# Performance work log

Hardware: AMD Instinct MI355X
Metric: run time of the kernel (lower is better)

Reference implementation:

```python
import jax, jax.numpy as jnp
import numpy as np

D_MODEL = 1024
NUM_HEADS = 16
HEAD_DIM = D_MODEL // NUM_HEADS


def setup_inputs() -> dict:
    key = jax.random.key(0)
    ks = jax.random.split(key, 11)
    B, S = 2, 2048
    s = 1.0 / np.sqrt(D_MODEL)
    return {
        "q": jax.random.normal(ks[0], (B, S, D_MODEL), jnp.float32),
        "k": jax.random.normal(ks[1], (B, S, D_MODEL), jnp.float32),
        "v": jax.random.normal(ks[2], (B, S, D_MODEL), jnp.float32),
        "Wq": jax.random.normal(ks[3], (D_MODEL, D_MODEL), jnp.float32) * s,
        "bq": jnp.zeros((D_MODEL,), jnp.float32),
        "Wk": jax.random.normal(ks[4], (D_MODEL, D_MODEL), jnp.float32) * s,
        "bk": jnp.zeros((D_MODEL,), jnp.float32),
        "Wv": jax.random.normal(ks[5], (D_MODEL, D_MODEL), jnp.float32) * s,
        "bv": jnp.zeros((D_MODEL,), jnp.float32),
        "Wo": jax.random.normal(ks[6], (D_MODEL, D_MODEL), jnp.float32) * s,
        "bo": jnp.zeros((D_MODEL,), jnp.float32),
    }


def _split_heads(x):
    B, S, _ = x.shape
    return x.reshape(B, S, NUM_HEADS, HEAD_DIM).transpose(0, 2, 1, 3)  # [B,H,S,Dh]


def reference(q, k, v, Wq, bq, Wk, bk, Wv, bv, Wo, bo):
    B, S, _ = q.shape
    qh = _split_heads(q @ Wq.T + bq)
    kh = _split_heads(k @ Wk.T + bk)
    vh = _split_heads(v @ Wv.T + bv)
    scale = 1.0 / jnp.sqrt(jnp.asarray(HEAD_DIM, qh.dtype))
    scores = jnp.einsum("bhqd,bhkd->bhqk", qh, kh) * scale  # [B,H,S,S]
    attn = jax.nn.softmax(scores, axis=-1)
    out = jnp.einsum("bhqk,bhkd->bhqd", attn, vh)
    out = out.transpose(0, 2, 1, 3).reshape(B, S, D_MODEL)
    return out @ Wo.T + bo
```

## Files before the change

kernel.cpp:

```cpp
#include <hip/hip_runtime.h>
#include <cstdint>
#include <cstddef>

#define DEVI __device__ __forceinline__

typedef short bf16x8 __attribute__((ext_vector_type(8)));
typedef short bf16x4 __attribute__((ext_vector_type(4)));
typedef float f32x4 __attribute__((ext_vector_type(4)));
typedef float f32x16 __attribute__((ext_vector_type(16)));
typedef unsigned short u16x4 __attribute__((ext_vector_type(4)));

constexpr int D_MODEL = 1024;
constexpr int HEADS = 16;
constexpr int DH = 64;
constexpr int SEQ = 2048;
constexpr int KDIM = 1024;

DEVI unsigned short f2bf(float f) {
  union { float f; unsigned u; } v; v.f = f;
  unsigned r = v.u + 0x7fffu + ((v.u >> 16) & 1u);
  return (unsigned short)(r >> 16);
}

DEVI unsigned pkbf(float a, float b) {
  return __builtin_amdgcn_perm(__float_as_uint(b), __float_as_uint(a), 0x07060302u);
}

DEVI void cp16(const void* g, void* l) {
  __builtin_amdgcn_global_load_lds(
      (const __attribute__((address_space(1))) void*)g,
      (__attribute__((address_space(3))) void*)l, 16, 0, 0);
}

#define BAR()        asm volatile("s_barrier" ::: "memory")
#define WAITVM(n)    asm volatile("s_waitcnt vmcnt(" #n ")" ::: "memory")

__global__ void __launch_bounds__(256) castall(
    const float* __restrict__ q, const float* __restrict__ k, const float* __restrict__ v,
    const float* __restrict__ Wq, const float* __restrict__ Wk,
    const float* __restrict__ Wv, const float* __restrict__ Wo,
    unsigned short* __restrict__ qb, unsigned short* __restrict__ kb, unsigned short* __restrict__ vb,
    unsigned short* __restrict__ Wqb, unsigned short* __restrict__ Wkb,
    unsigned short* __restrict__ Wvb, unsigned short* __restrict__ Wob) {
  int bid = blockIdx.x;
  const float* s; unsigned short* d; int off;
  if (bid < 12288) {
    int w = bid >> 12; off = bid & 4095;
    s = (w == 0) ? q : ((w == 1) ? k : v);
    d = (w == 0) ? qb : ((w == 1) ? kb : vb);
  } else {
    int w = (bid - 12288) >> 10; off = bid & 1023;
    s = (w == 0) ? Wq : ((w == 1) ? Wk : ((w == 2) ? Wv : Wo));
    d = (w == 0) ? Wqb : ((w == 1) ? Wkb : ((w == 2) ? Wvb : Wob));
  }
  int i = (off * 256 + threadIdx.x) * 4;
  float4 x = *(const float4*)(s + i);
  u16x4 o; o[0] = f2bf(x.x); o[1] = f2bf(x.y); o[2] = f2bf(x.z); o[3] = f2bf(x.w);
  *(u16x4*)(d + i) = o;
}

__global__ void __launch_bounds__(256) qkv_gemm(
    const unsigned short* __restrict__ qb, const unsigned short* __restrict__ kb,
    const unsigned short* __restrict__ vb,
    const unsigned short* __restrict__ Wqb, const unsigned short* __restrict__ Wkb,
    const unsigned short* __restrict__ Wvb,
    const float* __restrict__ bq, const float* __restrict__ bk, const float* __restrict__ bv,
    unsigned short* __restrict__ Qh, unsigned short* __restrict__ Kh,
    unsigned short* __restrict__ Vt, float qscale) {
  __shared__ unsigned short As[3][128 * 32];
  __shared__ unsigned short Bs[3][128 * 32];
  const int bid = blockIdx.x, seg = bid >> 8, inner = bid & 255;
  const int bm = inner & 31, bn = inner >> 5;
  const unsigned short* A = (seg == 0) ? qb : ((seg == 1) ? kb : vb);
  const unsigned short* W = (seg == 0) ? Wqb : ((seg == 1) ? Wkb : Wvb);
  const float* bias = (seg == 0) ? bq : ((seg == 1) ? bk : bv);
  unsigned short* O = (seg == 0) ? Qh : ((seg == 1) ? Kh : Vt);
  const float oscale = (seg == 0) ? qscale : 1.0f;
  const int mode = (seg == 2) ? 1 : 0;

  const int tid = threadIdx.x, lane = tid & 63, wave = tid >> 6;
  const int l16 = lane & 15, quad = lane >> 4;
  const int wm = (wave >> 1) * 64, wn = (wave & 1) * 64;
  const int sw = (l16 >> 1) & 3;
  f32x4 acc[4][4] = {};

  const int r0 = tid >> 2, p0 = tid & 3;
  const int c0 = (p0 ^ ((r0 >> 1) & 3)) * 8;
  const int r1 = (256 + tid) >> 2;
  const int c1 = (p0 ^ ((r1 >> 1) & 3)) * 8;
  const unsigned short* Arow0 = A + (size_t)(bm * 128 + r0) * KDIM + c0;
  const unsigned short* Arow1 = A + (size_t)(bm * 128 + r1) * KDIM + c1;
  const unsigned short* Wrow0 = W + (size_t)(bn * 128 + r0) * KDIM + c0;
  const unsigned short* Wrow1 = W + (size_t)(bn * 128 + r1) * KDIM + c1;

#define QKV_ISSUE(K0, P)                                    \
  do {                                                      \
    cp16(Arow0 + (K0), &As[P][tid * 8]);                    \
    cp16(Arow1 + (K0), &As[P][(256 + tid) * 8]);            \
    cp16(Wrow0 + (K0), &Bs[P][tid * 8]);                    \
    cp16(Wrow1 + (K0), &Bs[P][(256 + tid) * 8]);            \
  } while (0)

#define QKV_COMPUTE(P)                                                             \
  do {                                                                             \
    bf16x8 af[4], bfr[4];                                                          \
    _Pragma("unroll") for (int t = 0; t < 4; ++t)                                  \
        af[t] = *(const bf16x8*)&As[P][(wm + t * 16 + l16) * 32 + ((quad ^ sw) * 8)]; \
    _Pragma("unroll") for (int t = 0; t < 4; ++t)                                  \
        bfr[t] = *(const bf16x8*)&Bs[P][(wn + t * 16 + l16) * 32 + ((quad ^ sw) * 8)]; \
    _Pragma("unroll") for (int i = 0; i < 4; ++i)                                  \
        _Pragma("unroll") for (int j = 0; j < 4; ++j)                              \
            acc[i][j] = __builtin_amdgcn_mfma_f32_16x16x32_bf16(af[i], bfr[j],     \
                                                                acc[i][j], 0, 0, 0); \
  } while (0)

  QKV_ISSUE(0, 0);
  QKV_ISSUE(32, 1);
  for (int k = 0; k < 30; k += 3) {
    BAR(); QKV_ISSUE((k + 2) * 32, 2); WAITVM(8); BAR(); QKV_COMPUTE(0);
    BAR(); QKV_ISSUE((k + 3) * 32, 0); WAITVM(8); BAR(); QKV_COMPUTE(1);
    BAR(); QKV_ISSUE((k + 4) * 32, 1); WAITVM(8); BAR(); QKV_COMPUTE(2);
  }
  WAITVM(4); BAR(); QKV_COMPUTE(0);
  WAITVM(0); BAR(); QKV_COMPUTE(1);

#pragma unroll
  for (int i = 0; i < 4; ++i) {
#pragma unroll
    for (int j = 0; j < 4; ++j) {
      const int col = bn * 128 + wn + j * 16 + l16;
      const float bv = bias[col];
#pragma unroll
      for (int r = 0; r < 4; ++r) {
        const int row = bm * 128 + wm + i * 16 + quad * 4 + r;
        const float val = (acc[i][j][r] + bv) * oscale;
        const int b = row >> 11, s = row & (SEQ - 1);
        const int h = col >> 6, d = col & (DH - 1);
        size_t idx;
        if (mode == 0) idx = ((size_t)(b * HEADS + h) * SEQ + s) * DH + d;
        else           idx = ((size_t)(b * HEADS + h) * DH + d) * SEQ + s;
        O[idx] = f2bf(val);
      }
    }
  }
#undef QKV_ISSUE
#undef QKV_COMPUTE
}

__global__ void __launch_bounds__(256) out_gemm(const unsigned short* __restrict__ AO,
                                                const unsigned short* __restrict__ Wob,
                                                const float* __restrict__ bo,
                                                float* __restrict__ out) {
  __shared__ unsigned short As[3][128 * 32];
  __shared__ unsigned short Bs[3][128 * 32];
  const int bid = blockIdx.x, bm = bid & 31, bn = bid >> 5;
  const int tid = threadIdx.x, lane = tid & 63, wave = tid >> 6;
  const int l16 = lane & 15, quad = lane >> 4;
  const int wm = (wave >> 1) * 64, wn = (wave & 1) * 64;
  const int sw = (l16 >> 1) & 3;
  f32x4 acc[4][4] = {};

  const int r0 = tid >> 2, p0 = tid & 3;
  const int c0 = (p0 ^ ((r0 >> 1) & 3)) * 8;
  const int r1 = (256 + tid) >> 2;
  const int c1 = (p0 ^ ((r1 >> 1) & 3)) * 8;
  const unsigned short* Arow0 = AO + (size_t)(bm * 128 + r0) * KDIM + c0;
  const unsigned short* Arow1 = AO + (size_t)(bm * 128 + r1) * KDIM + c1;
  const unsigned short* Wrow0 = Wob + (size_t)(bn * 128 + r0) * KDIM + c0;
  const unsigned short* Wrow1 = Wob + (size_t)(bn * 128 + r1) * KDIM + c1;

#define OUT_ISSUE(K0, P)                                    \
  do {                                                      \
    cp16(Arow0 + (K0), &As[P][tid * 8]);                    \
    cp16(Arow1 + (K0), &As[P][(256 + tid) * 8]);            \
    cp16(Wrow0 + (K0), &Bs[P][tid * 8]);                    \
    cp16(Wrow1 + (K0), &Bs[P][(256 + tid) * 8]);            \
  } while (0)

#define OUT_COMPUTE(P)                                                             \
  do {                                                                             \
    bf16x8 af[4], bfr[4];                                                          \
    _Pragma("unroll") for (int t = 0; t < 4; ++t)                                  \
        af[t] = *(const bf16x8*)&As[P][(wm + t * 16 + l16) * 32 + ((quad ^ sw) * 8)]; \
    _Pragma("unroll") for (int t = 0; t < 4; ++t)                                  \
        bfr[t] = *(const bf16x8*)&Bs[P][(wn + t * 16 + l16) * 32 + ((quad ^ sw) * 8)]; \
    _Pragma("unroll") for (int i = 0; i < 4; ++i)                                  \
        _Pragma("unroll") for (int j = 0; j < 4; ++j)                              \
            acc[i][j] = __builtin_amdgcn_mfma_f32_16x16x32_bf16(af[i], bfr[j],     \
                                                                acc[i][j], 0, 0, 0); \
  } while (0)

  OUT_ISSUE(0, 0);
  OUT_ISSUE(32, 1);
  for (int k = 0; k < 30; k += 3) {
    BAR(); OUT_ISSUE((k + 2) * 32, 2); WAITVM(8); BAR(); OUT_COMPUTE(0);
    BAR(); OUT_ISSUE((k + 3) * 32, 0); WAITVM(8); BAR(); OUT_COMPUTE(1);
    BAR(); OUT_ISSUE((k + 4) * 32, 1); WAITVM(8); BAR(); OUT_COMPUTE(2);
  }
  WAITVM(4); BAR(); OUT_COMPUTE(0);
  WAITVM(0); BAR(); OUT_COMPUTE(1);

#pragma unroll
  for (int i = 0; i < 4; ++i)
#pragma unroll
    for (int j = 0; j < 4; ++j) {
      const int col = bn * 128 + wn + j * 16 + l16;
      const float bv = bo[col];
#pragma unroll
      for (int r = 0; r < 4; ++r) {
        const int row = bm * 128 + wm + i * 16 + quad * 4 + r;
        out[(size_t)row * D_MODEL + col] = acc[i][j][r] + bv;
      }
    }
#undef OUT_ISSUE
#undef OUT_COMPUTE
}

__global__ void __launch_bounds__(256, 1) attn(const unsigned short* __restrict__ Qh,
                                               const unsigned short* __restrict__ Kh,
                                               const unsigned short* __restrict__ Vt,
                                               unsigned short* __restrict__ AO) {
  __shared__ __align__(16) char smem[65536];

  const int bid = blockIdx.x;
  const int qt = bid >> 5, head = bid & 31, b = head >> 4, h = head & 15;
  const int tid = threadIdx.x;
  const int lane = tid & 63, wave = tid >> 6;
  const int wq = wave >> 1, wk = wave & 1;
  const int l31 = lane & 31, hh = lane >> 5;

  const unsigned short* Qhead = Qh + (size_t)(b * HEADS + h) * SEQ * DH;
  const unsigned short* Khead = Kh + (size_t)(b * HEADS + h) * SEQ * DH;
  const unsigned short* Vhead = Vt + (size_t)(b * HEADS + h) * DH * SEQ;

  const int qrow0 = qt * 128 + wq * 64 + l31;
  bf16x8 aq0[4], aq1[4];
#pragma unroll
  for (int it = 0; it < 4; ++it) {
    aq0[it] = *(const bf16x8*)&Qhead[(size_t)qrow0 * DH + it * 16 + hh * 8];
    aq1[it] = *(const bf16x8*)&Qhead[(size_t)(qrow0 + 32) * DH + it * 16 + hh * 8];
  }

  f32x16 oacc0[2] = {}, oacc1[2] = {};
  float lsum0 = 0.f, lsum1 = 0.f;

#define ATT_STAGE(KC, P)                                                      \
  do {                                                                        \
    unsigned short* Ksp = (unsigned short*)(smem + (P) * 32768);              \
    unsigned short* Vsp = (unsigned short*)(smem + (P) * 32768 + 16384);      \
    _Pragma("unroll") for (int c = 0; c < 4; ++c) {                           \
      int s = c * 256 + tid;                                                  \
      int row = s >> 3, pblk = s & 7;                                         \
      int jb = pblk ^ (row & 7);                                              \
      cp16(Khead + (size_t)((KC) * 128 + row) * DH + jb * 8, &Ksp[s * 8]);    \
    }                                                                         \
    _Pragma("unroll") for (int c = 0; c < 4; ++c) {                           \
      int s = c * 256 + tid;                                                  \
      int d = s >> 4, pblk = s & 15;                                          \
      int jb = pblk ^ (d & 7);                                                \
      cp16(Vhead + (size_t)d * SEQ + (KC) * 128 + jb * 8, &Vsp[s * 8]);       \
    }                                                                         \
  } while (0)

#define ATT_SOFTMAX(SA, PB, LSUM)                                             \
  do {                                                                        \
    float p[16];                                                              \
    _Pragma("unroll") for (int r = 0; r < 16; ++r) {                          \
      p[r] = __builtin_amdgcn_exp2f((SA)[r]);                                 \
      (LSUM) += p[r];                                                         \
    }                                                                         \
    _Pragma("unroll") for (int c = 0; c < 2; ++c) {                           \
      unsigned x0 = pkbf(p[8 * c + 0], p[8 * c + 1]);                         \
      unsigned x1 = pkbf(p[8 * c + 2], p[8 * c + 3]);                         \
      unsigned y0 = pkbf(p[8 * c + 4], p[8 * c + 5]);                         \
      unsigned y1 = pkbf(p[8 * c + 6], p[8 * c + 7]);                         \
      asm("v_permlane32_swap_b32 %0, %1" : "+v"(x0), "+v"(y0));               \
      asm("v_permlane32_swap_b32 %0, %1" : "+v"(x1), "+v"(y1));               \
      union { unsigned u[4]; bf16x8 s; } pbu;                                 \
      pbu.u[0] = x0; pbu.u[1] = x1; pbu.u[2] = y0; pbu.u[3] = y1;             \
      (PB)[c] = pbu.s;                                                        \
    }                                                                         \
  } while (0)

#define ATT_COMPUTE(P)                                                        \
  do {                                                                        \
    const unsigned short* Ksp = (const unsigned short*)(smem + (P) * 32768);  \
    const unsigned short* Vsp =                                               \
        (const unsigned short*)(smem + (P) * 32768 + 16384);                  \
    __builtin_amdgcn_s_setprio(1);                                            \
    _Pragma("unroll") for (int sub = 0; sub < 2; ++sub) {                     \
      const int key = sub * 64 + wk * 32 + l31;                               \
      bf16x8 ak[4];                                                           \
      _Pragma("unroll") for (int it = 0; it < 4; ++it) {                      \
        const int sblk = (2 * it + hh) ^ (key & 7);                           \
        ak[it] = *(const bf16x8*)&Ksp[key * 64 + sblk * 8];                   \
      }                                                                       \
      bf16x8 pb0[2], pb1[2];                                                  \
      {                                                                       \
        f32x16 sa = {};                                                       \
        _Pragma("unroll") for (int it = 0; it < 4; ++it)                      \
          sa = __builtin_amdgcn_mfma_f32_32x32x16_bf16(ak[it], aq0[it], sa,   \
                                                       0, 0, 0);              \
        ATT_SOFTMAX(sa, pb0, lsum0);                                          \
      }                                                                       \
      {                                                                       \
        f32x16 sa = {};                                                       \
        _Pragma("unroll") for (int it = 0; it < 4; ++it)                      \
          sa = __builtin_amdgcn_mfma_f32_32x32x16_bf16(ak[it], aq1[it], sa,   \
                                                       0, 0, 0);              \
        ATT_SOFTMAX(sa, pb1, lsum1);                                          \
      }                                                                       \
      _Pragma("unroll") for (int c = 0; c < 2; ++c) {                         \
        const int K8 = sub * 8 + wk * 4 + 2 * c + hh;                         \
        _Pragma("unroll") for (int dh2 = 0; dh2 < 2; ++dh2) {                 \
          const int d = dh2 * 32 + l31;                                       \
          const int sv = K8 ^ (d & 7);                                        \
          bf16x8 av = *(const bf16x8*)&Vsp[d * 128 + sv * 8];                 \
          oacc0[dh2] = __builtin_amdgcn_mfma_f32_32x32x16_bf16(av, pb0[c],    \
                                                               oacc0[dh2],   \
                                                               0, 0, 0);     \
          oacc1[dh2] = __builtin_amdgcn_mfma_f32_32x32x16_bf16(av, pb1[c],    \
                                                               oacc1[dh2],   \
                                                               0, 0, 0);     \
        }                                                                     \
      }                                                                       \
    }                                                                         \
    __builtin_amdgcn_s_setprio(0);                                            \
  } while (0)

  ATT_STAGE(0, 0);
  for (int kc = 0; kc < 16; ++kc) {
    WAITVM(0);
    BAR();
    if (kc < 15) ATT_STAGE(kc + 1, (kc + 1) & 1);
    ATT_COMPUTE(kc & 1);
    BAR();
  }

  lsum0 += __shfl_xor(lsum0, 32);
  lsum1 += __shfl_xor(lsum1, 32);

  float* epiF = (float*)smem;
  float* lbuf = (float*)(smem + 16384);
  unsigned short* Oq = (unsigned short*)(smem + 17408);

#define ATT_EPI(OACC, LSUM, SET)                                              \
  do {                                                                        \
    if (lane < 32) lbuf[wave * 32 + l31] = (LSUM);                            \
    if (wk == 1) {                                                            \
      _Pragma("unroll") for (int dh2 = 0; dh2 < 2; ++dh2)                     \
        _Pragma("unroll") for (int r = 0; r < 16; ++r) {                      \
          const int d = dh2 * 32 + (r & 3) + 8 * (r >> 2) + 4 * hh;           \
          epiF[wq * 2048 + d * 32 + l31] = (OACC)[dh2][r];                    \
        }                                                                     \
    }                                                                         \
    __syncthreads();                                                          \
    if (wk == 0) {                                                            \
      const float linv = 1.0f / ((LSUM) + lbuf[(wq * 2 + 1) * 32 + l31]);     \
      _Pragma("unroll") for (int dh2 = 0; dh2 < 2; ++dh2) {                   \
        _Pragma("unroll") for (int r = 0; r < 16; r += 2) {                   \
          const int d = dh2 * 32 + (r & 3) + 8 * (r >> 2) + 4 * hh;           \
          const float v0 =                                                    \
              ((OACC)[dh2][r] + epiF[wq * 2048 + d * 32 + l31]) * linv;       \
          const float v1 =                                                    \
              ((OACC)[dh2][r + 1] + epiF[wq * 2048 + (d + 1) * 32 + l31]) *   \
              linv;                                                           \
          *(unsigned*)&Oq[wq * 2176 + l31 * 68 + d] = pkbf(v0, v1);           \
        }                                                                     \
      }                                                                       \
    }                                                                         \
    __syncthreads();                                                          \
    {                                                                         \
      const int qloc = tid >> 2, d0 = (tid & 3) * 16;                         \
      const int base = (qloc >> 5) * 2176 + (qloc & 31) * 68 + d0;            \
      unsigned u[8];                                                          \
      _Pragma("unroll") for (int i = 0; i < 8; ++i)                           \
        u[i] = *(const unsigned*)&Oq[base + i * 2];                           \
      const int row = qt * 128 + (qloc >> 5) * 64 + (SET) * 32 + (qloc & 31); \
      unsigned short* dst =                                                   \
          AO + ((size_t)(b * SEQ + row)) * D_MODEL + h * 64 + d0;             \
      *(uint4*)dst       = make_uint4(u[0], u[1], u[2], u[3]);                \
      *(uint4*)(dst + 8) = make_uint4(u[4], u[5], u[6], u[7]);                \
    }                                                                         \
  } while (0)

  ATT_EPI(oacc0, lsum0, 0);
  __syncthreads();
  ATT_EPI(oacc1, lsum1, 1);

#undef ATT_STAGE
#undef ATT_SOFTMAX
#undef ATT_COMPUTE
#undef ATT_EPI
}

extern "C" void kernel_launch(void* const* d_in, const int* in_sizes, int n_in,
                              void* d_out, int out_size, void* d_ws, size_t ws_size,
                              hipStream_t stream) {
  const float* q  = (const float*)d_in[0];
  const float* k  = (const float*)d_in[1];
  const float* v  = (const float*)d_in[2];
  const float* Wq = (const float*)d_in[3];
  const float* bq = (const float*)d_in[4];
  const float* Wk = (const float*)d_in[5];
  const float* bk = (const float*)d_in[6];
  const float* Wv = (const float*)d_in[7];
  const float* bv = (const float*)d_in[8];
  const float* Wo = (const float*)d_in[9];
  const float* bo = (const float*)d_in[10];
  float* out = (float*)d_out;

  char* ws = (char*)d_ws;
  const size_t MB = 1ull << 20;
  unsigned short* qb  = (unsigned short*)(ws + 0 * MB);
  unsigned short* kb  = (unsigned short*)(ws + 8 * MB);
  unsigned short* vb  = (unsigned short*)(ws + 16 * MB);
  unsigned short* Wqb = (unsigned short*)(ws + 24 * MB);
  unsigned short* Wkb = (unsigned short*)(ws + 26 * MB);
  unsigned short* Wvb = (unsigned short*)(ws + 28 * MB);
  unsigned short* Wob = (unsigned short*)(ws + 30 * MB);
  unsigned short* Qh  = (unsigned short*)(ws + 32 * MB);
  unsigned short* Kh  = (unsigned short*)(ws + 40 * MB);
  unsigned short* Vt  = (unsigned short*)(ws + 48 * MB);
  unsigned short* AO  = (unsigned short*)(ws + 56 * MB);

  castall<<<16384, 256, 0, stream>>>(q, k, v, Wq, Wk, Wv, Wo,
                                     qb, kb, vb, Wqb, Wkb, Wvb, Wob);

  const float qscale = 0.125f * 1.44269504088896f;
  qkv_gemm<<<768, 256, 0, stream>>>(qb, kb, vb, Wqb, Wkb, Wvb, bq, bk, bv,
                                    Qh, Kh, Vt, qscale);

  attn<<<512, 256, 0, stream>>>(Qh, Kh, Vt, AO);

  out_gemm<<<256, 256, 0, stream>>>(AO, Wob, bo, out);
}
```

Baseline: 222.3 us.

## Fuse fp32-to-bf16 activation cast into QKV GEMM A-tile loads

The separate cast pass over the q/k/v activations is removed. The QKV GEMM now reads fp32 activations straight into registers, converts them to bf16 and writes them to LDS, while weights still use async global-to-LDS copies. The pipeline changes from three-stage async buffering to two-stage register-staged double buffering, with full vmcnt/lgkmcnt waits each step. This saves a full write and re-read of the bf16 activations, but the GEMM now reads twice as many A bytes and overlaps loads less.

```diff
diff --git a/kernel.cpp b/kernel.cpp
--- a/kernel.cpp
+++ b/kernel.cpp
@@ -34,25 +34,17 @@
 
 #define BAR()        asm volatile("s_barrier" ::: "memory")
 #define WAITVM(n)    asm volatile("s_waitcnt vmcnt(" #n ")" ::: "memory")
+#define WAITLG()     asm volatile("s_waitcnt lgkmcnt(0)" ::: "memory")
 
 __global__ void __launch_bounds__(256) castall(
-    const float* __restrict__ q, const float* __restrict__ k, const float* __restrict__ v,
     const float* __restrict__ Wq, const float* __restrict__ Wk,
     const float* __restrict__ Wv, const float* __restrict__ Wo,
-    unsigned short* __restrict__ qb, unsigned short* __restrict__ kb, unsigned short* __restrict__ vb,
     unsigned short* __restrict__ Wqb, unsigned short* __restrict__ Wkb,
     unsigned short* __restrict__ Wvb, unsigned short* __restrict__ Wob) {
   int bid = blockIdx.x;
-  const float* s; unsigned short* d; int off;
-  if (bid < 12288) {
-    int w = bid >> 12; off = bid & 4095;
-    s = (w == 0) ? q : ((w == 1) ? k : v);
-    d = (w == 0) ? qb : ((w == 1) ? kb : vb);
-  } else {
-    int w = (bid - 12288) >> 10; off = bid & 1023;
-    s = (w == 0) ? Wq : ((w == 1) ? Wk : ((w == 2) ? Wv : Wo));
-    d = (w == 0) ? Wqb : ((w == 1) ? Wkb : ((w == 2) ? Wvb : Wob));
-  }
+  int w = bid >> 10, off = bid & 1023;
+  const float* s = (w == 0) ? Wq : ((w == 1) ? Wk : ((w == 2) ? Wv : Wo));
+  unsigned short* d = (w == 0) ? Wqb : ((w == 1) ? Wkb : ((w == 2) ? Wvb : Wob));
   int i = (off * 256 + threadIdx.x) * 4;
   float4 x = *(const float4*)(s + i);
   u16x4 o; o[0] = f2bf(x.x); o[1] = f2bf(x.y); o[2] = f2bf(x.z); o[3] = f2bf(x.w);
@@ -60,18 +52,18 @@
 }
 
 __global__ void __launch_bounds__(256) qkv_gemm(
-    const unsigned short* __restrict__ qb, const unsigned short* __restrict__ kb,
-    const unsigned short* __restrict__ vb,
+    const float* __restrict__ qf, const float* __restrict__ kf,
+    const float* __restrict__ vf,
     const unsigned short* __restrict__ Wqb, const unsigned short* __restrict__ Wkb,
     const unsigned short* __restrict__ Wvb,
     const float* __restrict__ bq, const float* __restrict__ bk, const float* __restrict__ bv,
     unsigned short* __restrict__ Qh, unsigned short* __restrict__ Kh,
     unsigned short* __restrict__ Vt, float qscale) {
-  __shared__ unsigned short As[3][128 * 32];
-  __shared__ unsigned short Bs[3][128 * 32];
+  __shared__ unsigned short As[2][128 * 32];
+  __shared__ unsigned short Bs[2][128 * 32];
   const int bid = blockIdx.x, seg = bid >> 8, inner = bid & 255;
   const int bm = inner & 31, bn = inner >> 5;
-  const unsigned short* A = (seg == 0) ? qb : ((seg == 1) ? kb : vb);
+  const float* A = (seg == 0) ? qf : ((seg == 1) ? kf : vf);
   const unsigned short* W = (seg == 0) ? Wqb : ((seg == 1) ? Wkb : Wvb);
   const float* bias = (seg == 0) ? bq : ((seg == 1) ? bk : bv);
   unsigned short* O = (seg == 0) ? Qh : ((seg == 1) ? Kh : Vt);
@@ -88,17 +80,40 @@
   const int c0 = (p0 ^ ((r0 >> 1) & 3)) * 8;
   const int r1 = (256 + tid) >> 2;
   const int c1 = (p0 ^ ((r1 >> 1) & 3)) * 8;
-  const unsigned short* Arow0 = A + (size_t)(bm * 128 + r0) * KDIM + c0;
-  const unsigned short* Arow1 = A + (size_t)(bm * 128 + r1) * KDIM + c1;
+  const float* Arow0 = A + (size_t)(bm * 128 + r0) * KDIM + c0;
+  const float* Arow1 = A + (size_t)(bm * 128 + r1) * KDIM + c1;
   const unsigned short* Wrow0 = W + (size_t)(bn * 128 + r0) * KDIM + c0;
   const unsigned short* Wrow1 = W + (size_t)(bn * 128 + r1) * KDIM + c1;
 
-#define QKV_ISSUE(K0, P)                                    \
-  do {                                                      \
-    cp16(Arow0 + (K0), &As[P][tid * 8]);                    \
-    cp16(Arow1 + (K0), &As[P][(256 + tid) * 8]);            \
-    cp16(Wrow0 + (K0), &Bs[P][tid * 8]);                    \
-    cp16(Wrow1 + (K0), &Bs[P][(256 + tid) * 8]);            \
+  float4 ra0, ra1, rb0, rb1;
+
+#define ALOAD(K0)                                            \
+  do {                                                       \
+    ra0 = *(const float4*)(Arow0 + (K0));                    \
+    ra1 = *(const float4*)(Arow0 + (K0) + 4);                \
+    rb0 = *(const float4*)(Arow1 + (K0));                    \
+    rb1 = *(const float4*)(Arow1 + (K0) + 4);                \
+  } while (0)
+
+#define ISSUEW(K0, P)                                        \
+  do {                                                       \
+    cp16(Wrow0 + (K0), &Bs[P][tid * 8]);                     \
+    cp16(Wrow1 + (K0), &Bs[P][(256 + tid) * 8]);             \
+  } while (0)
+
+#define AWRITE(P)                                            \
+  do {                                                       \
+    union { u16x4 h[2]; bf16x8 v8; } ua, ub;                 \
+    ua.h[0][0] = f2bf(ra0.x); ua.h[0][1] = f2bf(ra0.y);      \
+    ua.h[0][2] = f2bf(ra0.z); ua.h[0][3] = f2bf(ra0.w);      \
+    ua.h[1][0] = f2bf(ra1.x); ua.h[1][1] = f2bf(ra1.y);      \
+    ua.h[1][2] = f2bf(ra1.z); ua.h[1][3] = f2bf(ra1.w);      \
+    ub.h[0][0] = f2bf(rb0.x); ub.h[0][1] = f2bf(rb0.y);      \
+    ub.h[0][2] = f2bf(rb0.z); ub.h[0][3] = f2bf(rb0.w);      \
+    ub.h[1][0] = f2bf(rb1.x); ub.h[1][1] = f2bf(rb1.y);      \
+    ub.h[1][2] = f2bf(rb1.z); ub.h[1][3] = f2bf(rb1.w);      \
+    *(bf16x8*)&As[P][tid * 8] = ua.v8;                       \
+    *(bf16x8*)&As[P][(256 + tid) * 8] = ub.v8;               \
   } while (0)
 
 #define QKV_COMPUTE(P)                                                             \
@@ -114,15 +129,24 @@
                                                                 acc[i][j], 0, 0, 0); \
   } while (0)
 
-  QKV_ISSUE(0, 0);
-  QKV_ISSUE(32, 1);
-  for (int k = 0; k < 30; k += 3) {
-    BAR(); QKV_ISSUE((k + 2) * 32, 2); WAITVM(8); BAR(); QKV_COMPUTE(0);
-    BAR(); QKV_ISSUE((k + 3) * 32, 0); WAITVM(8); BAR(); QKV_COMPUTE(1);
-    BAR(); QKV_ISSUE((k + 4) * 32, 1); WAITVM(8); BAR(); QKV_COMPUTE(2);
+  ALOAD(0); ISSUEW(0, 0);
+  WAITVM(0);
+  AWRITE(0);
+  WAITLG(); BAR();
+
+  for (int k = 0; k < 30; k += 2) {
+    ALOAD((k + 1) * 32); ISSUEW((k + 1) * 32, 1);
+    QKV_COMPUTE(0);
+    WAITVM(0); AWRITE(1); WAITLG(); BAR();
+
+    ALOAD((k + 2) * 32); ISSUEW((k + 2) * 32, 0);
+    QKV_COMPUTE(1);
+    WAITVM(0); AWRITE(0); WAITLG(); BAR();
   }
-  WAITVM(4); BAR(); QKV_COMPUTE(0);
-  WAITVM(0); BAR(); QKV_COMPUTE(1);
+  ALOAD(31 * 32); ISSUEW(31 * 32, 1);
+  QKV_COMPUTE(0);
+  WAITVM(0); AWRITE(1); WAITLG(); BAR();
+  QKV_COMPUTE(1);
 
 #pragma unroll
   for (int i = 0; i < 4; ++i) {
@@ -143,7 +167,9 @@
       }
     }
   }
-#undef QKV_ISSUE
+#undef ALOAD
+#undef ISSUEW
+#undef AWRITE
 #undef QKV_COMPUTE
 }
 
@@ -412,9 +438,6 @@
 
   char* ws = (char*)d_ws;
   const size_t MB = 1ull << 20;
-  unsigned short* qb  = (unsigned short*)(ws + 0 * MB);
-  unsigned short* kb  = (unsigned short*)(ws + 8 * MB);
-  unsigned short* vb  = (unsigned short*)(ws + 16 * MB);
   unsigned short* Wqb = (unsigned short*)(ws + 24 * MB);
   unsigned short* Wkb = (unsigned short*)(ws + 26 * MB);
   unsigned short* Wvb = (unsigned short*)(ws + 28 * MB);
@@ -424,11 +447,10 @@
   unsigned short* Vt  = (unsigned short*)(ws + 48 * MB);
   unsigned short* AO  = (unsigned short*)(ws + 56 * MB);
 
-  castall<<<16384, 256, 0, stream>>>(q, k, v, Wq, Wk, Wv, Wo,
-                                     qb, kb, vb, Wqb, Wkb, Wvb, Wob);
+  castall<<<4096, 256, 0, stream>>>(Wq, Wk, Wv, Wo, Wqb, Wkb, Wvb, Wob);
 
   const float qscale = 0.125f * 1.44269504088896f;
-  qkv_gemm<<<768, 256, 0, stream>>>(qb, kb, vb, Wqb, Wkb, Wvb, bq, bk, bv,
+  qkv_gemm<<<768, 256, 0, stream>>>(q, k, v, Wqb, Wkb, Wvb, bq, bk, bv,
                                     Qh, Kh, Vt, qscale);
 
   attn<<<512, 256, 0, stream>>>(Qh, Kh, Vt, AO);
```

New measurement: 252.1 us. +13.4%, slower.
